# Performance work log

Measured on AMD Instinct MI355X. Metric: run time of the kernel, lower is better.

The kernel has to match this reference:

```python
import jax, jax.numpy as jnp
import numpy as np

D_MODEL = 512
DEPTH = 2
D_STATE = 16
D_CONV = 4
EXPAND = 2
D_INNER = EXPAND * D_MODEL
DT_RANK = (D_MODEL + 15) // 16  # ceil(d_model/16) = 32
B_SZ = 8
SEQ = 2048


def setup_inputs() -> dict:
    key = jax.random.key(0)
    ks = jax.random.split(key, 8)
    s = 0.02
    A0 = jnp.log(jnp.broadcast_to(jnp.arange(1, D_STATE + 1, dtype=jnp.float32),
                                  (DEPTH, D_INNER, D_STATE)))
    return {
        "x": jax.random.normal(ks[0], (B_SZ, SEQ, D_MODEL), jnp.float32),
        "ln_w": jnp.ones((DEPTH, D_MODEL), jnp.float32),
        "ln_b": jnp.zeros((DEPTH, D_MODEL), jnp.float32),
        "in_proj_w": jax.random.normal(ks[1], (DEPTH, 2 * D_INNER, D_MODEL), jnp.float32) * s,
        "conv_w": jax.random.normal(ks[2], (DEPTH, D_INNER, 1, D_CONV), jnp.float32) * s,
        "conv_b": jnp.zeros((DEPTH, D_INNER), jnp.float32),
        "x_proj_w": jax.random.normal(ks[3], (DEPTH, DT_RANK + 2 * D_STATE, D_INNER), jnp.float32) * s,
        "dt_proj_w": jax.random.normal(ks[4], (DEPTH, D_INNER, DT_RANK), jnp.float32) * s,
        "dt_proj_b": jax.random.uniform(ks[5], (DEPTH, D_INNER), jnp.float32, -4.0, -2.0),
        "A_log": A0,
        "D_param": jnp.ones((DEPTH, D_INNER), jnp.float32),
        "out_proj_w": jax.random.normal(ks[6], (DEPTH, D_MODEL, D_INNER), jnp.float32) * s,
    }


def _layer_norm(x, w, b):
    mu = x.mean(-1, keepdims=True)
    var = ((x - mu) ** 2).mean(-1, keepdims=True)
    return (x - mu) * jax.lax.rsqrt(var + 1e-5) * w + b


def _mamba_block(x, in_w, cw, cb, xp_w, dtw, dtb, A_log, Dp, ow):
    B = x.shape[0]
    # input projection -> x branch and gate z
    xz = jnp.einsum('bld,ed->ble', x, in_w)          # [B,L,2*d_inner]
    xi, z = jnp.split(xz, 2, axis=-1)
    # depthwise causal conv1d over time
    xc = jnp.transpose(xi, (0, 2, 1))                 # [B,d_inner,L]
    xc = jax.lax.conv_general_dilated(
        xc, cw, (1,), [(D_CONV - 1, 0)],
        dimension_numbers=('NCH', 'OIH', 'NCH'),
        feature_group_count=D_INNER)
    xc = xc + cb[None, :, None]
    xi = jax.nn.silu(jnp.transpose(xc, (0, 2, 1)))    # [B,L,d_inner]
    # input-dependent dt, B, C
    dbc = jnp.einsum('ble,fe->blf', xi, xp_w)         # [B,L,dt_rank+2*d_state]
    dt = dbc[..., :DT_RANK]
    Bm = dbc[..., DT_RANK:DT_RANK + D_STATE]
    Cm = dbc[..., DT_RANK + D_STATE:]
    delta = jax.nn.softplus(jnp.einsum('blr,er->ble', dt, dtw) + dtb)  # [B,L,d_inner]
    A = -jnp.exp(A_log)                               # [d_inner,d_state]

    def step(h, ins):
        d_t, B_t, C_t, u_t = ins                      # [B,E],[B,N],[B,N],[B,E]
        dA = jnp.exp(d_t[..., None] * A)              # [B,E,N]
        h = dA * h + (d_t * u_t)[..., None] * B_t[:, None, :]
        y = jnp.einsum('ben,bn->be', h, C_t)
        return h, y

    h0 = jnp.zeros((B, D_INNER, D_STATE), x.dtype)
    ins = (jnp.transpose(delta, (1, 0, 2)),
           jnp.transpose(Bm, (1, 0, 2)),
           jnp.transpose(Cm, (1, 0, 2)),
           jnp.transpose(xi, (1, 0, 2)))
    _, ys = jax.lax.scan(step, h0, ins)               # ys: [L,B,d_inner]
    y = jnp.transpose(ys, (1, 0, 2)) + xi * Dp        # skip term D*u
    y = y * jax.nn.silu(z)                            # gate
    return jnp.einsum('ble,de->bld', y, ow)           # out projection


def reference(x, ln_w, ln_b, in_proj_w, conv_w, conv_b, x_proj_w,
              dt_proj_w, dt_proj_b, A_log, D_param, out_proj_w):
    for i in range(DEPTH):
        x = x + _mamba_block(_layer_norm(x, ln_w[i], ln_b[i]),
                             in_proj_w[i], conv_w[i], conv_b[i], x_proj_w[i],
                             dt_proj_w[i], dt_proj_b[i], A_log[i], D_param[i],
                             out_proj_w[i])
    return x
```

## Files before the change

kernel.cpp:

```cpp
#include <hip/hip_runtime.h>
#include <hip/hip_bf16.h>
#include <math.h>

#define B_SZ   8
#define SEQ    2048
#define DMODEL 512
#define DEPTH  2
#define DSTATE 16
#define DCONV  4
#define DINNER 1024
#define DTRANK 32
#define ROWS   (B_SZ * SEQ)
#define DBCW   (DTRANK + 2 * DSTATE)

typedef unsigned short u16;
typedef float f32x4 __attribute__((ext_vector_type(4)));
typedef short bf16x8 __attribute__((ext_vector_type(8)));

__device__ __forceinline__ float silu_f(float v) {
    return v * __builtin_amdgcn_rcpf(1.f + __expf(-v));
}
__device__ __forceinline__ float softplus_f(float s) {
    return (s > 20.f) ? s : __logf(1.f + __expf(s));
}
__device__ __forceinline__ u16 f2b(float v) {
    __hip_bfloat16 h = __float2bfloat16(v);
    return *(u16*)&h;
}
__device__ __forceinline__ float b2f(u16 v) {
    __hip_bfloat16 h;
    *(u16*)&h = v;
    return __bfloat162float(h);
}
__device__ __forceinline__ float sum16(float x) {
    x += __int_as_float(__builtin_amdgcn_update_dpp(0, __float_as_int(x), 0x121, 0xf, 0xf, true));
    x += __int_as_float(__builtin_amdgcn_update_dpp(0, __float_as_int(x), 0x122, 0xf, 0xf, true));
    x += __int_as_float(__builtin_amdgcn_update_dpp(0, __float_as_int(x), 0x124, 0xf, 0xf, true));
    x += __int_as_float(__builtin_amdgcn_update_dpp(0, __float_as_int(x), 0x128, 0xf, 0xf, true));
    return x;
}

__device__ __forceinline__ void load_lds16(const void* g, void* l) {
    __builtin_amdgcn_global_load_lds(
        (const __attribute__((address_space(1))) unsigned int*)g,
        (__attribute__((address_space(3))) unsigned int*)l, 16, 0, 0);
}

#define N_INW  (2 * DINNER * DMODEL)
#define N_OUTW (DMODEL * DINNER)
#define N_XW   (DBCW * DINNER)
__global__ __launch_bounds__(256) void conv_weights(const float* __restrict__ iw,
                                                    const float* __restrict__ ow,
                                                    const float* __restrict__ xw,
                                                    u16* __restrict__ inwbf,
                                                    u16* __restrict__ outwbf,
                                                    u16* __restrict__ xwbf) {
    int i = blockIdx.x * 256 + threadIdx.x;
    if (i < N_INW) inwbf[i] = f2b(iw[i]);
    else if (i < N_INW + N_OUTW) outwbf[i - N_INW] = f2b(ow[i - N_INW]);
    else if (i < N_INW + N_OUTW + N_XW) xwbf[i - N_INW - N_OUTW] = f2b(xw[i - N_INW - N_OUTW]);
}

__global__ __launch_bounds__(256) void ln_kernel(const float* __restrict__ x,
                                                 const float* __restrict__ w,
                                                 const float* __restrict__ b,
                                                 u16* __restrict__ out) {
    int r = blockIdx.x;
    int tid = threadIdx.x;
    const float* xr = x + (size_t)r * DMODEL;
    float2 v = *(const float2*)(xr + tid * 2);
    float s = v.x + v.y;
    float s2 = v.x * v.x + v.y * v.y;
    #pragma unroll
    for (int off = 1; off < 64; off <<= 1) {
        s  += __shfl_xor(s, off);
        s2 += __shfl_xor(s2, off);
    }
    __shared__ float ws[4], ws2[4];
    int wid = tid >> 6, lane = tid & 63;
    if (lane == 0) { ws[wid] = s; ws2[wid] = s2; }
    __syncthreads();
    float ts = ws[0] + ws[1] + ws[2] + ws[3];
    float ts2 = ws2[0] + ws2[1] + ws2[2] + ws2[3];
    float mean = ts * (1.f / DMODEL);
    float var = ts2 * (1.f / DMODEL) - mean * mean;
    float inv = rsqrtf(var + 1e-5f);
    out[(size_t)r * DMODEL + tid * 2]     = f2b((v.x - mean) * inv * w[tid * 2] + b[tid * 2]);
    out[(size_t)r * DMODEL + tid * 2 + 1] = f2b((v.y - mean) * inv * w[tid * 2 + 1] + b[tid * 2 + 1]);
}

__global__ __launch_bounds__(256) void gemm_in(const u16* __restrict__ A,
                                               const u16* __restrict__ W,
                                               u16* __restrict__ xi_re,
                                               u16* __restrict__ sz_re) {
    __shared__ u16 As[128 * 32];
    __shared__ u16 Bs[128 * 32];
    const int K = DMODEL, N = 2 * DINNER;
    int tid = threadIdx.x;
    int wave = tid >> 6, lane = tid & 63;
    int wm = (wave >> 1) * 64, wn = (wave & 1) * 64;
    int m0 = blockIdx.y * 128, n0 = blockIdx.x * 128;
    int srow = lane >> 2, sseg = lane & 3;
    const u16* Ag = A + (size_t)(m0 + wave * 32 + srow) * K + sseg * 8;
    const u16* Wg = W + (size_t)(n0 + wave * 32 + srow) * K + sseg * 8;
    u16* Asw = As + wave * 32 * 32;
    u16* Bsw = Bs + wave * 32 * 32;

    f32x4 acc[4][4] = {};
    int col = lane & 15, quad = lane >> 4;

    for (int k0 = 0; k0 < K; k0 += 32) {
        __syncthreads();
        load_lds16(Ag + k0, Asw);
        load_lds16(Ag + k0 + (size_t)16 * K, Asw + 16 * 32);
        load_lds16(Wg + k0, Bsw);
        load_lds16(Wg + k0 + (size_t)16 * K, Bsw + 16 * 32);
        __syncthreads();
        bf16x8 af[4], bfr[4];
        #pragma unroll
        for (int i = 0; i < 4; ++i) {
            af[i]  = *(const bf16x8*)(As + (wm + i * 16 + col) * 32 + quad * 8);
            bfr[i] = *(const bf16x8*)(Bs + (wn + i * 16 + col) * 32 + quad * 8);
        }
        #pragma unroll
        for (int i = 0; i < 4; ++i)
            #pragma unroll
            for (int j = 0; j < 4; ++j)
                acc[i][j] = __builtin_amdgcn_mfma_f32_16x16x32_bf16(af[i], bfr[j], acc[i][j], 0, 0, 0);
    }
    bool is_z = (n0 >= DINNER);
    u16* dst = is_z ? sz_re : xi_re;
    int nb = n0 & (DINNER - 1);
    #pragma unroll
    for (int i = 0; i < 4; ++i) {
        int gm_base = m0 + wm + i * 16 + quad * 4;
        #pragma unroll
        for (int j = 0; j < 4; ++j) {
            int gn = nb + wn + j * 16 + col;
            #pragma unroll
            for (int r = 0; r < 4; ++r) {
                float v = acc[i][j][r];
                if (is_z) v = silu_f(v);
                dst[(size_t)(gm_base + r) * DINNER + gn] = f2b(v);
            }
        }
    }
}

__global__ __launch_bounds__(256) void gemm_out(const u16* __restrict__ A,
                                                const u16* __restrict__ W,
                                                const float* __restrict__ res,
                                                float* __restrict__ C) {
    __shared__ u16 As[128 * 32];
    __shared__ u16 Bs[128 * 32];
    const int K = DINNER, N = DMODEL;
    int tid = threadIdx.x;
    int wave = tid >> 6, lane = tid & 63;
    int wm = (wave >> 1) * 64, wn = (wave & 1) * 64;
    int m0 = blockIdx.y * 128, n0 = blockIdx.x * 128;
    int srow = lane >> 2, sseg = lane & 3;
    const u16* Ag = A + (size_t)(m0 + wave * 32 + srow) * K + sseg * 8;
    const u16* Wg = W + (size_t)(n0 + wave * 32 + srow) * K + sseg * 8;
    u16* Asw = As + wave * 32 * 32;
    u16* Bsw = Bs + wave * 32 * 32;

    f32x4 acc[4][4] = {};
    int col = lane & 15, quad = lane >> 4;

    for (int k0 = 0; k0 < K; k0 += 32) {
        __syncthreads();
        load_lds16(Ag + k0, Asw);
        load_lds16(Ag + k0 + (size_t)16 * K, Asw + 16 * 32);
        load_lds16(Wg + k0, Bsw);
        load_lds16(Wg + k0 + (size_t)16 * K, Bsw + 16 * 32);
        __syncthreads();
        bf16x8 af[4], bfr[4];
        #pragma unroll
        for (int i = 0; i < 4; ++i) {
            af[i]  = *(const bf16x8*)(As + (wm + i * 16 + col) * 32 + quad * 8);
            bfr[i] = *(const bf16x8*)(Bs + (wn + i * 16 + col) * 32 + quad * 8);
        }
        #pragma unroll
        for (int i = 0; i < 4; ++i)
            #pragma unroll
            for (int j = 0; j < 4; ++j)
                acc[i][j] = __builtin_amdgcn_mfma_f32_16x16x32_bf16(af[i], bfr[j], acc[i][j], 0, 0, 0);
    }
    #pragma unroll
    for (int i = 0; i < 4; ++i) {
        int gm_base = m0 + wm + i * 16 + quad * 4;
        #pragma unroll
        for (int j = 0; j < 4; ++j) {
            int gn = n0 + wn + j * 16 + col;
            #pragma unroll
            for (int r = 0; r < 4; ++r) {
                size_t off = (size_t)(gm_base + r) * N + gn;
                C[off] = acc[i][j][r] + res[off];
            }
        }
    }
}

__global__ __launch_bounds__(256) void gemm_xp_bf16(const u16* __restrict__ A,
                                                    const u16* __restrict__ W,
                                                    float* __restrict__ C) {
    __shared__ u16 As[128 * 32];
    __shared__ u16 Bs[64 * 32];
    int tid = threadIdx.x;
    int wave = tid >> 6, lane = tid & 63;
    int m0 = blockIdx.x * 128;
    int wm = wave * 32;
    int srow = lane >> 2, sseg = lane & 3;
    const u16* Ag = A + (size_t)(m0 + wm + srow) * DINNER + sseg * 8;
    const u16* Wg = W + (size_t)(wave * 16 + srow) * DINNER + sseg * 8;
    u16* Asw = As + wave * 32 * 32;
    u16* Bsw = Bs + wave * 16 * 32;

    f32x4 acc[2][4] = {};
    int col = lane & 15, quad = lane >> 4;

    for (int k0 = 0; k0 < DINNER; k0 += 32) {
        __syncthreads();
        load_lds16(Ag + k0, Asw);
        load_lds16(Ag + k0 + (size_t)16 * DINNER, Asw + 16 * 32);
        load_lds16(Wg + k0, Bsw);
        __syncthreads();
        bf16x8 af[2], bfr[4];
        #pragma unroll
        for (int i = 0; i < 2; ++i)
            af[i] = *(const bf16x8*)(As + (wm + i * 16 + col) * 32 + quad * 8);
        #pragma unroll
        for (int j = 0; j < 4; ++j)
            bfr[j] = *(const bf16x8*)(Bs + (j * 16 + col) * 32 + quad * 8);
        #pragma unroll
        for (int i = 0; i < 2; ++i)
            #pragma unroll
            for (int j = 0; j < 4; ++j)
                acc[i][j] = __builtin_amdgcn_mfma_f32_16x16x32_bf16(af[i], bfr[j], acc[i][j], 0, 0, 0);
    }
    #pragma unroll
    for (int i = 0; i < 2; ++i) {
        int gm_base = m0 + wm + i * 16 + quad * 4;
        #pragma unroll
        for (int j = 0; j < 4; ++j) {
            int gn = j * 16 + col;
            #pragma unroll
            for (int r = 0; r < 4; ++r)
                C[(size_t)(gm_base + r) * DBCW + gn] = acc[i][j][r];
        }
    }
}

__global__ __launch_bounds__(256) void u_t_kernel(const u16* __restrict__ xi_re,
                                                  const u16* __restrict__ sz_re,
                                                  const float* __restrict__ cw,
                                                  const float* __restrict__ cb,
                                                  u16* __restrict__ ut,
                                                  u16* __restrict__ u_re,
                                                  u16* __restrict__ szt) {
    __shared__ float xt[67][65];
    __shared__ u16 uo[64][70];
    __shared__ u16 szo[64][70];
    int tid = threadIdx.x;
    int t0 = blockIdx.x * 64, e0 = blockIdx.y * 64, b = blockIdx.z;
    int er = tid & 63, rr = tid >> 6;
    for (int it = 0; it < 17; ++it) {
        int row = it * 4 + rr;
        if (row < 67) {
            int t = t0 + row - 3;
            xt[row][er] = (t >= 0) ? b2f(xi_re[((size_t)b * SEQ + t) * DINNER + e0 + er]) : 0.f;
        }
    }
    #pragma unroll
    for (int it = 0; it < 16; ++it) {
        int row = it * 4 + rr;
        szo[er][row] = sz_re[((size_t)b * SEQ + t0 + row) * DINNER + e0 + er];
    }
    __syncthreads();
    {
        int e = tid & 63, tg = tid >> 6;
        float4 w4 = *(const float4*)(cw + (e0 + e) * 4);
        float cbe = cb[e0 + e];
        int tl0 = tg * 16;
        float x3 = xt[tl0][e], x2 = xt[tl0 + 1][e], x1 = xt[tl0 + 2][e];
        #pragma unroll
        for (int i = 0; i < 16; ++i) {
            float x0 = xt[tl0 + i + 3][e];
            float u = silu_f(cbe + w4.x * x3 + w4.y * x2 + w4.z * x1 + w4.w * x0);
            x3 = x2; x2 = x1; x1 = x0;
            u16 ub = f2b(u);
            uo[e][tl0 + i] = ub;
            u_re[((size_t)b * SEQ + t0 + tl0 + i) * DINNER + e0 + e] = ub;
        }
    }
    __syncthreads();
    {
        int tl = tid & 63, eg = tid >> 6;
        #pragma unroll
        for (int i = 0; i < 16; ++i) {
            int ee = eg * 16 + i;
            ut[((size_t)b * DINNER + e0 + ee) * SEQ + t0 + tl] = uo[ee][tl];
            szt[((size_t)b * DINNER + e0 + ee) * SEQ + t0 + tl] = szo[ee][tl];
        }
    }
}

__global__ __launch_bounds__(256) void delta_bct_kernel(const float* __restrict__ dbc,
                                                        const float* __restrict__ dtw,
                                                        const float* __restrict__ dtb,
                                                        u16* __restrict__ dlt,
                                                        u16* __restrict__ Bt,
                                                        u16* __restrict__ Ct) {
    __shared__ float wl[64 * 32];
    __shared__ float bl[64];
    int tid = threadIdx.x;
    int e0 = blockIdx.x * 64, t0 = blockIdx.y * 256, b = blockIdx.z;
    for (int i = tid; i < 64 * 32; i += 256) wl[i] = dtw[(size_t)e0 * DTRANK + i];
    if (tid < 64) bl[tid] = dtb[e0 + tid];
    float dreg[32];
    const float* dp = dbc + (size_t)(b * SEQ + t0 + tid) * DBCW;
    #pragma unroll
    for (int k = 0; k < 32; k += 4) {
        float4 v = *(const float4*)(dp + k);
        dreg[k] = v.x; dreg[k + 1] = v.y; dreg[k + 2] = v.z; dreg[k + 3] = v.w;
    }
    __syncthreads();
    for (int ep = 0; ep < 64; ++ep) {
        float s = bl[ep];
        #pragma unroll
        for (int k = 0; k < 32; ++k) s += dreg[k] * wl[ep * 32 + k];
        dlt[((size_t)b * DINNER + e0 + ep) * SEQ + t0 + tid] = f2b(softplus_f(s));
    }
    if (blockIdx.x == 0) {
        int t = t0 + tid;
        const float* dp2 = dbc + (size_t)(b * SEQ + t) * DBCW + DTRANK;
        #pragma unroll
        for (int nn = 0; nn < DSTATE; ++nn) {
            Bt[((size_t)b * DSTATE + nn) * SEQ + t] = f2b(dp2[nn]);
            Ct[((size_t)b * DSTATE + nn) * SEQ + t] = f2b(dp2[DSTATE + nn]);
        }
    }
}

#define SCHUNK 8

__global__ __launch_bounds__(256, 2) void scan_fused(u16* __restrict__ y_re,
                                                     const u16* __restrict__ ut,
                                                     const u16* __restrict__ dlt,
                                                     const u16* __restrict__ Bt,
                                                     const u16* __restrict__ Ct,
                                                     const u16* __restrict__ szt,
                                                     const float* __restrict__ Alog,
                                                     const float* __restrict__ Dp) {
    int tid = threadIdx.x;
    int pair = tid >> 4, n = tid & 15;
    int blk = blockIdx.x;
    int b = blk >> 6;
    int e = ((blk & 63) << 4) + pair;
    float a = -__expf(Alog[e * DSTATE + n]);
    float dpe = Dp[e];
    const u16* urow  = ut  + ((size_t)b * DINNER + e) * SEQ;
    const u16* dlrow = dlt + ((size_t)b * DINNER + e) * SEQ;
    const u16* szrow = szt + ((size_t)b * DINNER + e) * SEQ;
    const u16* Brow  = Bt + ((size_t)b * DSTATE + n) * SEQ;
    const u16* Crow  = Ct + ((size_t)b * DSTATE + n) * SEQ;
    u16* yrow = y_re + (size_t)b * SEQ * DINNER + e;

    float h = 0.f;
    bf16x8 Au, Adl, AB, AC, Asz, Bu, Bdl, BB, BC, Bsz;

    auto load = [&](int c, bf16x8& u8, bf16x8& d8, bf16x8& b8, bf16x8& c8, bf16x8& s8) {
        u8 = *(const bf16x8*)(urow + c * SCHUNK);
        d8 = *(const bf16x8*)(dlrow + c * SCHUNK);
        b8 = *(const bf16x8*)(Brow + c * SCHUNK);
        c8 = *(const bf16x8*)(Crow + c * SCHUNK);
        s8 = *(const bf16x8*)(szrow + c * SCHUNK);
    };
    auto proc = [&](int c, bf16x8 u8, bf16x8 d8, bf16x8 b8, bf16x8 c8, bf16x8 s8) {
        u16* yp_ = yrow + (size_t)c * SCHUNK * DINNER;
        #pragma unroll
        for (int j = 0; j < SCHUNK; ++j) {
            float uf = b2f((u16)u8[j]);
            float dl = b2f((u16)d8[j]);
            float dA = __expf(dl * a);
            h = dA * h + (dl * uf) * b2f((u16)b8[j]);
            float yp = sum16(h * b2f((u16)c8[j]));
            if (n == 0)
                yp_[(size_t)j * DINNER] = f2b((yp + uf * dpe) * b2f((u16)s8[j]));
        }
    };

    const int nc = SEQ / SCHUNK;
    load(0, Au, Adl, AB, AC, Asz);
    for (int c = 0; c < nc; c += 2) {
        load(c + 1, Bu, Bdl, BB, BC, Bsz);
        proc(c, Au, Adl, AB, AC, Asz);
        if (c + 2 < nc) load(c + 2, Au, Adl, AB, AC, Asz);
        proc(c + 1, Bu, Bdl, BB, BC, Bsz);
    }
}

extern "C" void kernel_launch(void* const* d_in, const int* in_sizes, int n_in,
                              void* d_out, int out_size, void* d_ws, size_t ws_size,
                              hipStream_t stream) {
    const float* x_in   = (const float*)d_in[0];
    const float* ln_w   = (const float*)d_in[1];
    const float* ln_b   = (const float*)d_in[2];
    const float* inw    = (const float*)d_in[3];
    const float* convw  = (const float*)d_in[4];
    const float* convb  = (const float*)d_in[5];
    const float* xpw    = (const float*)d_in[6];
    const float* dtw    = (const float*)d_in[7];
    const float* dtb    = (const float*)d_in[8];
    const float* Alog   = (const float*)d_in[9];
    const float* Dp     = (const float*)d_in[10];
    const float* outw   = (const float*)d_in[11];
    float* out = (float*)d_out;

    char* p = (char*)d_ws;
    u16* xi_re = (u16*)p;               p += (size_t)ROWS * DINNER * 2;
    u16* sz_re = (u16*)p;               p += (size_t)ROWS * DINNER * 2;
    u16* y_re  = (u16*)p;               p += (size_t)ROWS * DINNER * 2;
    float* dbc = (float*)p;             p += (size_t)ROWS * DBCW * 4;
    u16* dlt   = (u16*)p;               p += (size_t)B_SZ * DINNER * SEQ * 2;
    u16* u_re  = dlt;
    u16* Bt    = (u16*)p;               p += (size_t)B_SZ * DSTATE * SEQ * 2;
    u16* xwbf  = Bt;
    u16* Ct    = (u16*)p;               p += (size_t)B_SZ * DSTATE * SEQ * 2;
    u16* ut    = (u16*)p;               p += (size_t)B_SZ * DINNER * SEQ * 2;
    u16* xnbf  = ut;
    u16* szt   = (u16*)p;               p += (size_t)B_SZ * DINNER * SEQ * 2;
    u16* inwbf = (u16*)p;               p += (size_t)N_INW * 2;
    u16* outwbf = (u16*)p;              p += (size_t)N_OUTW * 2;

    const dim3 blk256(256);
    const int n_conv = N_INW + N_OUTW + N_XW;

    for (int i = 0; i < DEPTH; ++i) {
        const float* x_cur = (i == 0) ? x_in : out;
        const float* lw  = ln_w  + (size_t)i * DMODEL;
        const float* lb  = ln_b  + (size_t)i * DMODEL;
        const float* iw  = inw   + (size_t)i * 2 * DINNER * DMODEL;
        const float* cw  = convw + (size_t)i * DINNER * DCONV;
        const float* cb  = convb + (size_t)i * DINNER;
        const float* xw  = xpw   + (size_t)i * DBCW * DINNER;
        const float* dw  = dtw   + (size_t)i * DINNER * DTRANK;
        const float* db  = dtb   + (size_t)i * DINNER;
        const float* Al  = Alog  + (size_t)i * DINNER * DSTATE;
        const float* Dpp = Dp    + (size_t)i * DINNER;
        const float* ow  = outw  + (size_t)i * DMODEL * DINNER;

        conv_weights<<<(n_conv + 255) / 256, blk256, 0, stream>>>(
            iw, ow, xw, inwbf, outwbf, xwbf);
        ln_kernel<<<ROWS, blk256, 0, stream>>>(x_cur, lw, lb, xnbf);
        gemm_in<<<dim3(2 * DINNER / 128, ROWS / 128), blk256, 0, stream>>>(
            xnbf, inwbf, xi_re, sz_re);
        u_t_kernel<<<dim3(SEQ / 64, DINNER / 64, B_SZ), blk256, 0, stream>>>(
            xi_re, sz_re, cw, cb, ut, u_re, szt);
        gemm_xp_bf16<<<ROWS / 128, blk256, 0, stream>>>(u_re, xwbf, dbc);
        delta_bct_kernel<<<dim3(DINNER / 64, SEQ / 256, B_SZ), blk256, 0, stream>>>(
            dbc, dw, db, dlt, Bt, Ct);
        scan_fused<<<(B_SZ * DINNER) / 16, blk256, 0, stream>>>(
            y_re, ut, dlt, Bt, Ct, szt, Al, Dpp);
        gemm_out<<<dim3(DMODEL / 128, ROWS / 128), blk256, 0, stream>>>(
            y_re, outwbf, x_cur, out);
    }
}
```

Baseline: 980.0 us.

## Spread scan output stores across state lanes and use exp2 in selective scan

The scan kernel now processes 16-step chunks. Each of the 16 state lanes keeps the output for the timestep matching its index and writes it once per chunk, so one lane no longer issues every store. The gate value is loaded as one scalar per lane instead of an 8-wide vector, and the decay exponent uses a prescaled exp2 intrinsic. This spreads global stores and gate loads across lanes and cuts per-step branching, at the cost of more registers for the doubled prefetch buffers, which may reduce occupancy.

```diff
diff --git a/kernel.cpp b/kernel.cpp
--- a/kernel.cpp
+++ b/kernel.cpp
@@ -95,7 +95,7 @@
                                                u16* __restrict__ sz_re) {
     __shared__ u16 As[128 * 32];
     __shared__ u16 Bs[128 * 32];
-    const int K = DMODEL, N = 2 * DINNER;
+    const int K = DMODEL;
     int tid = threadIdx.x;
     int wave = tid >> 6, lane = tid & 63;
     int wm = (wave >> 1) * 64, wn = (wave & 1) * 64;
@@ -342,7 +342,7 @@
     }
 }
 
-#define SCHUNK 8
+#define SCHUNK 16
 
 __global__ __launch_bounds__(256, 2) void scan_fused(u16* __restrict__ y_re,
                                                      const u16* __restrict__ ut,
@@ -357,46 +357,55 @@
     int blk = blockIdx.x;
     int b = blk >> 6;
     int e = ((blk & 63) << 4) + pair;
-    float a = -__expf(Alog[e * DSTATE + n]);
+    float a2 = -__expf(Alog[e * DSTATE + n]) * 1.44269504f;
     float dpe = Dp[e];
     const u16* urow  = ut  + ((size_t)b * DINNER + e) * SEQ;
     const u16* dlrow = dlt + ((size_t)b * DINNER + e) * SEQ;
     const u16* szrow = szt + ((size_t)b * DINNER + e) * SEQ;
     const u16* Brow  = Bt + ((size_t)b * DSTATE + n) * SEQ;
     const u16* Crow  = Ct + ((size_t)b * DSTATE + n) * SEQ;
-    u16* yrow = y_re + (size_t)b * SEQ * DINNER + e;
+    u16* ystore = y_re + ((size_t)b * SEQ + n) * DINNER + e;
 
     float h = 0.f;
-    bf16x8 Au, Adl, AB, AC, Asz, Bu, Bdl, BB, BC, Bsz;
-
-    auto load = [&](int c, bf16x8& u8, bf16x8& d8, bf16x8& b8, bf16x8& c8, bf16x8& s8) {
-        u8 = *(const bf16x8*)(urow + c * SCHUNK);
-        d8 = *(const bf16x8*)(dlrow + c * SCHUNK);
-        b8 = *(const bf16x8*)(Brow + c * SCHUNK);
-        c8 = *(const bf16x8*)(Crow + c * SCHUNK);
-        s8 = *(const bf16x8*)(szrow + c * SCHUNK);
+    bf16x8 Au0, Au1, Adl0, Adl1, AB0, AB1, AC0, AC1;
+    bf16x8 Bu0, Bu1, Bdl0, Bdl1, BB0, BB1, BC0, BC1;
+    float Asz, Bsz;
+
+    auto load = [&](int c, bf16x8& u0, bf16x8& u1, bf16x8& d0, bf16x8& d1,
+                    bf16x8& b0, bf16x8& b1, bf16x8& c0, bf16x8& c1, float& sz) {
+        u0 = *(const bf16x8*)(urow + c * SCHUNK);
+        u1 = *(const bf16x8*)(urow + c * SCHUNK + 8);
+        d0 = *(const bf16x8*)(dlrow + c * SCHUNK);
+        d1 = *(const bf16x8*)(dlrow + c * SCHUNK + 8);
+        b0 = *(const bf16x8*)(Brow + c * SCHUNK);
+        b1 = *(const bf16x8*)(Brow + c * SCHUNK + 8);
+        c0 = *(const bf16x8*)(Crow + c * SCHUNK);
+        c1 = *(const bf16x8*)(Crow + c * SCHUNK + 8);
+        sz = b2f(szrow[c * SCHUNK + n]);
     };
-    auto proc = [&](int c, bf16x8 u8, bf16x8 d8, bf16x8 b8, bf16x8 c8, bf16x8 s8) {
-        u16* yp_ = yrow + (size_t)c * SCHUNK * DINNER;
+    auto proc = [&](int c, bf16x8 u0, bf16x8 u1, bf16x8 d0, bf16x8 d1,
+                    bf16x8 b0, bf16x8 b1, bf16x8 c0, bf16x8 c1, float sz) {
+        float keep = 0.f;
         #pragma unroll
         for (int j = 0; j < SCHUNK; ++j) {
-            float uf = b2f((u16)u8[j]);
-            float dl = b2f((u16)d8[j]);
-            float dA = __expf(dl * a);
-            h = dA * h + (dl * uf) * b2f((u16)b8[j]);
-            float yp = sum16(h * b2f((u16)c8[j]));
-            if (n == 0)
-                yp_[(size_t)j * DINNER] = f2b((yp + uf * dpe) * b2f((u16)s8[j]));
-        }
+            float uf = b2f((u16)((j < 8) ? u0[j] : u1[j - 8]));
+            float dl = b2f((u16)((j < 8) ? d0[j] : d1[j - 8]));
+            float dA = __builtin_amdgcn_exp2f(dl * a2);
+            h = dA * h + (dl * uf) * b2f((u16)((j < 8) ? b0[j] : b1[j - 8]));
+            float yp = sum16(h * b2f((u16)((j < 8) ? c0[j] : c1[j - 8])));
+            float yg = yp + uf * dpe;
+            keep = (n == j) ? yg : keep;
+        }
+        ystore[(size_t)c * SCHUNK * DINNER] = f2b(keep * sz);
     };
 
     const int nc = SEQ / SCHUNK;
-    load(0, Au, Adl, AB, AC, Asz);
+    load(0, Au0, Au1, Adl0, Adl1, AB0, AB1, AC0, AC1, Asz);
     for (int c = 0; c < nc; c += 2) {
-        load(c + 1, Bu, Bdl, BB, BC, Bsz);
-        proc(c, Au, Adl, AB, AC, Asz);
-        if (c + 2 < nc) load(c + 2, Au, Adl, AB, AC, Asz);
-        proc(c + 1, Bu, Bdl, BB, BC, Bsz);
+        load(c + 1, Bu0, Bu1, Bdl0, Bdl1, BB0, BB1, BC0, BC1, Bsz);
+        proc(c, Au0, Au1, Adl0, Adl1, AB0, AB1, AC0, AC1, Asz);
+        if (c + 2 < nc) load(c + 2, Au0, Au1, Adl0, Adl1, AB0, AB1, AC0, AC1, Asz);
+        proc(c + 1, Bu0, Bu1, Bdl0, Bdl1, BB0, BB1, BC0, BC1, Bsz);
     }
 }
 
```

Measured after the change: 853.9 us. -12.9%, faster.
